# Performance work log

Measured on AMD Instinct MI355X. Metric: run time of the kernel, lower is better.

## Reference

```python
import jax, jax.numpy as jnp
import numpy as np

B, N, C = 8, 8192, 64
P, K = 2048, 16
C_IN = 2 * C + 6   # 134: concat(diff, center) of (feat ++ xyz)
H1, H2 = 64, 128
EPS = 1e-5


def setup_inputs() -> dict:
    key = jax.random.key(0)
    ks = jax.random.split(key, 16)
    inp = {
        "xyz": jax.random.normal(ks[0], (B, N, 3), dtype=jnp.float32),
        "feat": jax.random.normal(ks[1], (B, C, N), dtype=jnp.float32),
        # SharedMLP layer 1: 1x1 conv + BN(eval) + ReLU
        "W1": jax.random.normal(ks[2], (H1, C_IN), dtype=jnp.float32) * (1.0 / np.sqrt(C_IN)),
        "b1": jnp.zeros((H1,), dtype=jnp.float32),
        "g1": jax.random.uniform(ks[3], (H1,), minval=0.5, maxval=1.5, dtype=jnp.float32),
        "be1": jax.random.normal(ks[4], (H1,), dtype=jnp.float32) * 0.1,
        "m1": jax.random.normal(ks[5], (H1,), dtype=jnp.float32) * 0.1,
        "v1": jax.random.uniform(ks[6], (H1,), minval=0.5, maxval=1.5, dtype=jnp.float32),
        # SharedMLP layer 2
        "W2": jax.random.normal(ks[7], (H2, H1), dtype=jnp.float32) * (1.0 / np.sqrt(H1)),
        "b2": jnp.zeros((H2,), dtype=jnp.float32),
        "g2": jax.random.uniform(ks[8], (H2,), minval=0.5, maxval=1.5, dtype=jnp.float32),
        "be2": jax.random.normal(ks[9], (H2,), dtype=jnp.float32) * 0.1,
        "m2": jax.random.normal(ks[10], (H2,), dtype=jnp.float32) * 0.1,
        "v2": jax.random.uniform(ks[11], (H2,), minval=0.5, maxval=1.5, dtype=jnp.float32),
        "npoints": P,
    }
    return inp


def _mlp_layer(x, W, b, g, be, m, v):
    # x: [b,p,k,cin] -> 1x1 conv (einsum) + eval-mode BN + ReLU
    y = jnp.einsum("bpkc,oc->bpko", x, W) + b
    y = g * (y - m) * jax.lax.rsqrt(v + EPS) + be
    return jax.nn.relu(y)


def reference(xyz, feat, W1, b1, g1, be1, m1, v1, W2, b2, g2, be2, m2, v2, npoints):
    p = npoints
    # Range sampling: take first p points
    new_xyz = xyz[:, :p]                       # [b,p,3]
    feat_t = jnp.swapaxes(feat, 1, 2)          # [b,n,c]
    feat_x = jnp.concatenate([feat_t, xyz], axis=-1)   # [b,n,c+3] (use_xyz)
    new_feat_x = feat_x[:, :p]                 # [b,p,c+3]
    # KNN via squared euclidean distance, expanded form to avoid [b,p,n,3]
    sq_q = jnp.sum(new_xyz * new_xyz, axis=-1)           # [b,p]
    sq_r = jnp.sum(xyz * xyz, axis=-1)                   # [b,n]
    dots = jnp.einsum("bpd,bnd->bpn", new_xyz, xyz)      # [b,p,n]
    d2 = sq_q[:, :, None] + sq_r[:, None, :] - 2.0 * dots
    _, idx = jax.lax.top_k(-d2, K)             # [b,p,k] nearest (ascending dist)
    # Gather neighbor features: [b,p,k,c+3]
    knn_feat = jax.vmap(lambda f, i: f[i])(feat_x, idx)
    tiled = jnp.broadcast_to(new_feat_x[:, :, None, :], knn_feat.shape)
    edge = jnp.concatenate([knn_feat - tiled, tiled], axis=-1)  # [b,p,k,2c+6]
    h = _mlp_layer(edge, W1, b1, g1, be1, m1, v1)
    h = _mlp_layer(h, W2, b2, g2, be2, m2, v2)              # [b,p,k,H2]
    new_feat = jnp.swapaxes(jnp.max(h, axis=2), 1, 2)       # [b,H2,p]
    sample_idx = jnp.broadcast_to(jnp.arange(p, dtype=jnp.int32), (xyz.shape[0], p))
    return new_xyz, new_feat, sample_idx
```

## Files before the change

kernel.cpp:

```cpp
#include <hip/hip_runtime.h>
#include <hip/hip_bf16.h>

#define BB 8
#define NN 8192
#define CC 64
#define PP 2048
#define KK 16
#define H1 64
#define H2 128
#define K2PAD 72

typedef float  f32x4 __attribute__((ext_vector_type(4)));
typedef short  s16x8 __attribute__((ext_vector_type(8)));

#define OFF_FXT   0u
#define OFF_PTS4  17825792u
#define OFF_W1P   20971520u
#define OFF_W2P   20996096u
#define OFF_C1    21014528u
#define OFF_C2    21014784u

#define FLTMAX 3.402823466e+38f

static __device__ __forceinline__ unsigned short bf16b(float v) {
    __hip_bfloat16 h = __float2bfloat16(v);
    return *reinterpret_cast<unsigned short*>(&h);
}
static __device__ __forceinline__ unsigned pk2(float a, float b) {
    return ((unsigned)bf16b(b) << 16) | (unsigned)bf16b(a);
}
static __device__ __forceinline__ s16x8 as8(uint4 v) {
    union { uint4 u; s16x8 s; } x; x.u = v; return x.s;
}
#define LDS_FENCE() asm volatile("s_waitcnt lgkmcnt(0)" ::: "memory")

__global__ __launch_bounds__(512) void k1_prep(const float* __restrict__ xyz,
                                               const float* __restrict__ feat,
                                               unsigned* __restrict__ fxtb,
                                               float4* __restrict__ pts4,
                                               float* __restrict__ out0,
                                               float* __restrict__ out2,
                                               const float* __restrict__ W1, const float* __restrict__ b1,
                                               const float* __restrict__ g1, const float* __restrict__ be1,
                                               const float* __restrict__ m1, const float* __restrict__ v1,
                                               const float* __restrict__ W2, const float* __restrict__ b2,
                                               const float* __restrict__ g2, const float* __restrict__ be2,
                                               const float* __restrict__ m2, const float* __restrict__ v2,
                                               unsigned short* __restrict__ w1p,
                                               unsigned short* __restrict__ w2p,
                                               float* __restrict__ c1, float* __restrict__ c2) {
    __shared__ float tile[72][65];
    if (blockIdx.x < 256 && threadIdx.x < 85) {
        int i = blockIdx.x * 85 + threadIdx.x;
        if (i < 6144) {
            int n = i / 96, c = i - n * 96;
            float s = g1[n] * rsqrtf(v1[n] + 1e-5f);
            w1p[n * 192 + c] = bf16b((c < 67) ? W1[n * 134 + c] * s : 0.f);
        } else if (i < 12288) {
            int j = i - 6144;
            int n = j / 96, c = j - n * 96;
            float s = g1[n] * rsqrtf(v1[n] + 1e-5f);
            w1p[n * 192 + 96 + c] =
                bf16b((c < 67) ? (W1[n * 134 + 67 + c] - W1[n * 134 + c]) * s : 0.f);
        } else if (i < 21504) {
            int j = i - 12288;
            int o = j / 72, k = j - o * 72;
            float s = g2[o] * rsqrtf(v2[o] + 1e-5f);
            w2p[j] = bf16b((k < 64) ? W2[o * 64 + k] * s : 0.f);
        } else if (i < 21568) {
            int l = i - 21504;
            float s = g1[l] * rsqrtf(v1[l] + 1e-5f);
            c1[l] = s * (b1[l] - m1[l]) + be1[l];
        } else if (i < 21696) {
            int p = i - 21568;
            float s = g2[p] * rsqrtf(v2[p] + 1e-5f);
            c2[p] = s * (b2[p] - m2[p]) + be2[p];
        }
    }
    int b  = blockIdx.x >> 7;
    int n0 = (blockIdx.x & 127) * 64;
    int tx = threadIdx.x & 63, ty = threadIdx.x >> 6;
    for (int c = ty; c < 72; c += 8) {
        float v;
        if (c < 64)       v = feat[((size_t)b * 64 + c) * NN + n0 + tx];
        else if (c < 67)  v = xyz[((size_t)b * NN + n0 + tx) * 3 + (c - 64)];
        else              v = 0.f;
        tile[c][tx] = v;
    }
    __syncthreads();
    size_t base = ((size_t)b * NN + n0) * 36;
    for (int e = threadIdx.x; e < 64 * 36; e += 512) {
        int nl = e / 36, c = e - nl * 36;
        fxtb[base + e] = pk2(tile[2 * c][nl], tile[2 * c + 1][nl]);
    }
    if (threadIdx.x < 64) {
        int n = n0 + threadIdx.x;
        float x = tile[64][threadIdx.x], y = tile[65][threadIdx.x], z = tile[66][threadIdx.x];
        pts4[(size_t)b * NN + n] = make_float4(x, y, z, x * x + y * y + z * z);
        if (n0 < PP) out2[b * PP + n] = (float)n;
    }
    if (n0 < PP) {
        for (int e = threadIdx.x; e < 64 * 3; e += 512) {
            int nl = e / 3, d = e - nl * 3;
            out0[((size_t)b * PP + n0 + nl) * 3 + d] = tile[64 + d][nl];
        }
    }
}

__global__ __launch_bounds__(1024, 1) void k23(const float4* __restrict__ pts4,
                                               const unsigned* __restrict__ fxtb,
                                               const unsigned short* __restrict__ w1p,
                                               const unsigned short* __restrict__ w2p,
                                               const float* __restrict__ c1,
                                               const float* __restrict__ c2,
                                               float* __restrict__ out1) {
    __shared__ __align__(16) char smem[131072];
    __shared__ float2 scratch[16][2][64];
    __shared__ int knnl[16][64];
    int lane = threadIdx.x & 63;
    int wv   = threadIdx.x >> 6;
    int b    = blockIdx.x & 7;
    int q0base = (blockIdx.x >> 3) * 64;
    size_t pb = (size_t)b * NN;

    {
        float4* stage = (float4*)smem;
        int q0 = q0base + wv * 4;

        float4 qc = make_float4(0.f, 0.f, 0.f, 0.f);
        if (lane < 4) qc = pts4[pb + q0 + lane];
        float qx2 = -2.f * qc.x, qy2 = -2.f * qc.y, qz2 = -2.f * qc.z;
        float bx[4], by[4], bz[4];
#pragma unroll
        for (int q = 0; q < 4; ++q) {
            bx[q] = __shfl(qx2, q); by[q] = __shfl(qy2, q); bz[q] = __shfl(qz2, q);
        }

#pragma unroll
        for (int i = 0; i < 8; ++i) {
            int p = i * 1024 + threadIdx.x;
            float4 v = pts4[pb + p];
            int r = p >> 6, c = p & 63;
            stage[(r << 6) | ((c + (r >> 1)) & 63)] = v;
        }
        __syncthreads();

        float m[4];
#pragma unroll
        for (int q = 0; q < 4; ++q) m[q] = FLTMAX;
#pragma unroll
        for (int rr = 0; rr < 2; ++rr) {
            int rowbase = (2 * lane + rr) << 6;
#pragma unroll
            for (int j8 = 0; j8 < 8; ++j8) {
                float4 cc[8];
#pragma unroll
                for (int i = 0; i < 8; ++i)
                    cc[i] = stage[rowbase | ((j8 * 8 + i + lane) & 63)];
#pragma unroll
                for (int q = 0; q < 4; ++q) {
                    float x = bx[q], y = by[q], z = bz[q];
#pragma unroll
                    for (int i = 0; i < 8; i += 2) {
                        float e0 = fmaf(z, cc[i].z, fmaf(y, cc[i].y, fmaf(x, cc[i].x, cc[i].w)));
                        float e1 = fmaf(z, cc[i+1].z, fmaf(y, cc[i+1].y, fmaf(x, cc[i+1].x, cc[i+1].w)));
                        m[q] = fminf(fminf(m[q], e0), e1);
                    }
                }
            }
        }

        float sv0 = m[0], sv1 = m[1], sv2 = m[2], sv3 = m[3];
#pragma unroll
        for (int k = 2; k <= 64; k <<= 1) {
#pragma unroll
            for (int j = k >> 1; j > 0; j >>= 1) {
                bool keepMin = (((lane & k) == 0) == ((lane & j) == 0));
                float p0 = __shfl_xor(sv0, j, 64);
                float p1 = __shfl_xor(sv1, j, 64);
                float p2 = __shfl_xor(sv2, j, 64);
                float p3 = __shfl_xor(sv3, j, 64);
                sv0 = keepMin ? fminf(sv0, p0) : fmaxf(sv0, p0);
                sv1 = keepMin ? fminf(sv1, p1) : fmaxf(sv1, p1);
                sv2 = keepMin ? fminf(sv2, p2) : fmaxf(sv2, p2);
                sv3 = keepMin ? fminf(sv3, p3) : fmaxf(sv3, p3);
            }
        }
        float T[4];
        T[0] = __shfl(sv0, 15, 64); T[1] = __shfl(sv1, 15, 64);
        T[2] = __shfl(sv2, 15, 64); T[3] = __shfl(sv3, 15, 64);

        unsigned long long below = (lane == 63) ? 0x7FFFFFFFFFFFFFFFull
                                                : ((1ull << lane) - 1ull);
#pragma unroll
        for (int pr = 0; pr < 4; pr += 2) {
            int Ms[2];
#pragma unroll
            for (int u = 0; u < 2; ++u) {
                int q = pr + u;
                float x = bx[q], y = by[q], z = bz[q], tq = T[q];
                unsigned long long rm = __ballot(m[q] <= tq);
                int cnt = 0;
                while (rm) {
                    int sl = __ffsll((long long)rm) - 1; rm &= rm - 1;
                    int phys = (lane + sl) & 63;
                    float4 c0 = stage[((2 * sl) << 6) | phys];
                    float4 c1v_ = stage[((2 * sl + 1) << 6) | phys];
                    float e0 = fmaf(z, c0.z, fmaf(y, c0.y, fmaf(x, c0.x, c0.w)));
                    float e1 = fmaf(z, c1v_.z, fmaf(y, c1v_.y, fmaf(x, c1v_.x, c1v_.w)));
                    unsigned long long b0 = __ballot(e0 <= tq);
                    if (e0 <= tq) {
                        int pos = cnt + __popcll(b0 & below);
                        if (pos < 64)
                            scratch[wv][u][pos] = make_float2(e0, __int_as_float(sl * 128 + lane));
                    }
                    cnt += __popcll(b0);
                    unsigned long long b1 = __ballot(e1 <= tq);
                    if (e1 <= tq) {
                        int pos = cnt + __popcll(b1 & below);
                        if (pos < 64)
                            scratch[wv][u][pos] = make_float2(e1, __int_as_float(sl * 128 + 64 + lane));
                    }
                    cnt += __popcll(b1);
                }
                Ms[u] = min(cnt, 64);
            }
            LDS_FENCE();
#pragma unroll
            for (int u = 0; u < 2; ++u) {
                int M = Ms[u];
                float2 own = scratch[wv][u][lane];
                float di = own.x; int ni = __float_as_int(own.y);
                int rank = 0;
                const float2* buf = &scratch[wv][u][0];
#pragma unroll 4
                for (int j = 0; j < M; ++j) {
                    float2 e = buf[j];
                    int nj = __float_as_int(e.y);
                    rank += (e.x < di || (e.x == di && nj < ni)) ? 1 : 0;
                }
                if (lane < M && rank < 16)
                    knnl[wv][(pr + u) * 16 + rank] = ni;
            }
            LDS_FENCE();
        }
    }

    int idxAll = knnl[wv][lane];

    __syncthreads();

    unsigned short* w1a   = (unsigned short*)smem;
    unsigned short* w2l   = (unsigned short*)(smem + 13312);
    unsigned short* h1all = (unsigned short*)(smem + 35840);
    float*          otile = (float*)(smem + 72704);
    int col = lane & 15, quad = lane >> 4;
    const uint4* fx4 = (const uint4*)fxtb;
    size_t rowb = (size_t)b * NN;

    {
        const unsigned* src1 = (const unsigned*)w1p;
        unsigned* d1 = (unsigned*)w1a;
        for (int t = threadIdx.x; t < 64 * 48; t += 1024) {
            int r = t / 48, c = t - r * 48;
            d1[r * 52 + c] = src1[r * 96 + c];
        }
        const unsigned* src2 = (const unsigned*)w2p;
        unsigned* d2 = (unsigned*)w2l;
        for (int t = threadIdx.x; t < 128 * 36; t += 1024) {
            int r = t / 36, c = t - r * 36;
            d2[r * 44 + c] = src2[r * 36 + c];
        }
    }

    f32x4 accq[4];
#pragma unroll
    for (int nt = 0; nt < 4; ++nt) accq[nt] = (f32x4){0.f, 0.f, 0.f, 0.f};
    {
        const uint4* rp = fx4 + (rowb + q0base + wv * 4 + col) * 9;
        uint4 qf0 = rp[quad];
        uint4 qf1 = rp[4 + quad];
        uint4 qf2 = rp[8];
        if (quad != 0) qf2 = make_uint4(0u, 0u, 0u, 0u);
        uint4 qf[3] = {qf0, qf1, qf2};
#pragma unroll
        for (int ks = 0; ks < 3; ++ks) {
            s16x8 a = as8(qf[ks]);
#pragma unroll
            for (int nt = 0; nt < 4; ++nt) {
                s16x8 bfr = *(const s16x8*)(w1p + (nt * 16 + col) * 192 + 96 + ks * 32 + quad * 8);
                accq[nt] = __builtin_amdgcn_mfma_f32_16x16x32_bf16(a, bfr, accq[nt], 0, 0, 0);
            }
        }
    }
    float qcc[4][4];
    {
        float c1v[4];
#pragma unroll
        for (int nt = 0; nt < 4; ++nt) c1v[nt] = c1[nt * 16 + col];
#pragma unroll
        for (int qi = 0; qi < 4; ++qi)
#pragma unroll
            for (int nt = 0; nt < 4; ++nt)
                qcc[qi][nt] = __shfl(accq[nt][qi], col, 64) + c1v[nt];
    }
    float c2v[8];
#pragma unroll
    for (int nt = 0; nt < 8; ++nt) c2v[nt] = c2[nt * 16 + col];

    __syncthreads();

    unsigned short* h1w = h1all + wv * (16 * K2PAD);

    uint4 af[2][3];
#define PREF(buf, qi_) {                                                      \
        int nidx_ = __shfl(idxAll, (qi_) * 16 + col, 64);                     \
        const uint4* rp_ = fx4 + (rowb + nidx_) * 9;                          \
        af[buf][0] = rp_[quad];                                               \
        af[buf][1] = rp_[4 + quad];                                           \
        uint4 f2_ = rp_[8];                                                   \
        af[buf][2] = (quad == 0) ? f2_ : make_uint4(0u, 0u, 0u, 0u); }

    PREF(0, 0);

#pragma unroll
    for (int qi = 0; qi < 4; ++qi) {
        const int cur = qi & 1;
        f32x4 acc1[4];
#pragma unroll
        for (int nt = 0; nt < 4; ++nt)
            acc1[nt] = (f32x4){qcc[qi][nt], qcc[qi][nt], qcc[qi][nt], qcc[qi][nt]};
#pragma unroll
        for (int ks = 0; ks < 3; ++ks) {
            s16x8 a = as8(af[cur][ks]);
#pragma unroll
            for (int nt = 0; nt < 4; ++nt) {
                s16x8 bfr = *(const s16x8*)(w1a + (nt * 16 + col) * 104 + ks * 32 + quad * 8);
                acc1[nt] = __builtin_amdgcn_mfma_f32_16x16x32_bf16(a, bfr, acc1[nt], 0, 0, 0);
            }
        }
        if (qi < 3) PREF(cur ^ 1, qi + 1);
#pragma unroll
        for (int nt = 0; nt < 4; ++nt)
#pragma unroll
            for (int rr = 0; rr < 4; ++rr)
                h1w[(quad * 4 + rr) * K2PAD + nt * 16 + col] = bf16b(fmaxf(acc1[nt][rr], 0.f));
        LDS_FENCE();
#pragma unroll
        for (int hf = 0; hf < 2; ++hf) {
            f32x4 acc2[4];
#pragma unroll
            for (int nt = 0; nt < 4; ++nt) acc2[nt] = (f32x4){0.f, 0.f, 0.f, 0.f};
#pragma unroll
            for (int ks = 0; ks < 2; ++ks) {
                s16x8 a2 = *(const s16x8*)(h1w + col * K2PAD + ks * 32 + quad * 8);
#pragma unroll
                for (int nt = 0; nt < 4; ++nt) {
                    s16x8 wf = *(const s16x8*)(w2l + ((hf * 4 + nt) * 16 + col) * 88 + ks * 32 + quad * 8);
                    acc2[nt] = __builtin_amdgcn_mfma_f32_16x16x32_bf16(a2, wf, acc2[nt], 0, 0, 0);
                }
            }
#pragma unroll
            for (int nt = 0; nt < 4; ++nt) {
                float m0 = fmaxf(fmaxf(acc2[nt][0], acc2[nt][1]), fmaxf(acc2[nt][2], acc2[nt][3]));
                m0 = fmaxf(m0 + c2v[hf * 4 + nt], 0.f);
                m0 = fmaxf(m0, __shfl_xor(m0, 16, 64));
                m0 = fmaxf(m0, __shfl_xor(m0, 32, 64));
                if (quad == 0)
                    otile[(wv * 4 + qi) * 130 + (hf * 4 + nt) * 16 + col] = m0;
            }
        }
        LDS_FENCE();
    }
    __syncthreads();
    for (int i = threadIdx.x; i < H2 * 64; i += 1024) {
        int ch = i >> 6, q = i & 63;
        out1[((size_t)(b * H2 + ch)) * PP + q0base + q] = otile[q * 130 + ch];
    }
#undef PREF
}

extern "C" void kernel_launch(void* const* d_in, const int* in_sizes, int n_in,
                              void* d_out, int out_size, void* d_ws, size_t ws_size,
                              hipStream_t stream) {
    const float* xyz  = (const float*)d_in[0];
    const float* feat = (const float*)d_in[1];
    const float* W1   = (const float*)d_in[2];
    const float* b1   = (const float*)d_in[3];
    const float* g1   = (const float*)d_in[4];
    const float* be1  = (const float*)d_in[5];
    const float* m1   = (const float*)d_in[6];
    const float* v1   = (const float*)d_in[7];
    const float* W2   = (const float*)d_in[8];
    const float* b2   = (const float*)d_in[9];
    const float* g2   = (const float*)d_in[10];
    const float* be2  = (const float*)d_in[11];
    const float* m2   = (const float*)d_in[12];
    const float* v2   = (const float*)d_in[13];

    char* ws = (char*)d_ws;
    unsigned*       fxtb = (unsigned*)(ws + OFF_FXT);
    float4*         pts4 = (float4*)(ws + OFF_PTS4);
    unsigned short* w1p  = (unsigned short*)(ws + OFF_W1P);
    unsigned short* w2p  = (unsigned short*)(ws + OFF_W2P);
    float*          c1   = (float*)(ws + OFF_C1);
    float*          c2   = (float*)(ws + OFF_C2);

    float* out0 = (float*)d_out;
    float* out1 = out0 + (size_t)BB * PP * 3;
    float* out2 = out1 + (size_t)BB * H2 * PP;

    hipLaunchKernelGGL(k1_prep, dim3(1024), dim3(512), 0, stream,
                       xyz, feat, fxtb, pts4, out0, out2,
                       W1, b1, g1, be1, m1, v1, W2, b2, g2, be2, m2, v2,
                       w1p, w2p, c1, c2);
    hipLaunchKernelGGL(k23, dim3(256), dim3(1024), 0, stream,
                       pts4, fxtb, w1p, w2p, c1, c2, out1);
}
```

Baseline: 153.5 us.

## Fuse prep and KNN/MLP kernels into one cooperative kernel with grid sync

Merges the preprocessing kernel into the main KNN+MLP kernel, launched cooperatively with 256 blocks. Each block transposes and packs its share of features to bf16 and prepares weights, then runs KNN, and a grid-wide sync placed before the MLP phase guarantees the packed data is visible. The pts4 buffer is dropped; points and their squared norms are recomputed from xyz directly. The second-layer A fragments are also hoisted out of the hf loop. The aim is to remove one kernel launch and to overlap the prep work with the KNN phase, at the cost of cooperative-launch constraints, a grid barrier, and strided 3-float xyz loads.

```diff
diff --git a/kernel.cpp b/kernel.cpp
--- a/kernel.cpp
+++ b/kernel.cpp
@@ -1,5 +1,8 @@
 #include <hip/hip_runtime.h>
 #include <hip/hip_bf16.h>
+#include <hip/hip_cooperative_groups.h>
+
+namespace cg = cooperative_groups;
 
 #define BB 8
 #define NN 8192
@@ -14,7 +17,6 @@
 typedef short  s16x8 __attribute__((ext_vector_type(8)));
 
 #define OFF_FXT   0u
-#define OFF_PTS4  17825792u
 #define OFF_W1P   20971520u
 #define OFF_W2P   20996096u
 #define OFF_C1    21014528u
@@ -34,101 +36,96 @@
 }
 #define LDS_FENCE() asm volatile("s_waitcnt lgkmcnt(0)" ::: "memory")
 
-__global__ __launch_bounds__(512) void k1_prep(const float* __restrict__ xyz,
-                                               const float* __restrict__ feat,
-                                               unsigned* __restrict__ fxtb,
-                                               float4* __restrict__ pts4,
-                                               float* __restrict__ out0,
-                                               float* __restrict__ out2,
-                                               const float* __restrict__ W1, const float* __restrict__ b1,
-                                               const float* __restrict__ g1, const float* __restrict__ be1,
-                                               const float* __restrict__ m1, const float* __restrict__ v1,
-                                               const float* __restrict__ W2, const float* __restrict__ b2,
-                                               const float* __restrict__ g2, const float* __restrict__ be2,
-                                               const float* __restrict__ m2, const float* __restrict__ v2,
-                                               unsigned short* __restrict__ w1p,
-                                               unsigned short* __restrict__ w2p,
-                                               float* __restrict__ c1, float* __restrict__ c2) {
-    __shared__ float tile[72][65];
-    if (blockIdx.x < 256 && threadIdx.x < 85) {
-        int i = blockIdx.x * 85 + threadIdx.x;
-        if (i < 6144) {
-            int n = i / 96, c = i - n * 96;
-            float s = g1[n] * rsqrtf(v1[n] + 1e-5f);
-            w1p[n * 192 + c] = bf16b((c < 67) ? W1[n * 134 + c] * s : 0.f);
-        } else if (i < 12288) {
-            int j = i - 6144;
-            int n = j / 96, c = j - n * 96;
-            float s = g1[n] * rsqrtf(v1[n] + 1e-5f);
-            w1p[n * 192 + 96 + c] =
-                bf16b((c < 67) ? (W1[n * 134 + 67 + c] - W1[n * 134 + c]) * s : 0.f);
-        } else if (i < 21504) {
-            int j = i - 12288;
-            int o = j / 72, k = j - o * 72;
-            float s = g2[o] * rsqrtf(v2[o] + 1e-5f);
-            w2p[j] = bf16b((k < 64) ? W2[o * 64 + k] * s : 0.f);
-        } else if (i < 21568) {
-            int l = i - 21504;
-            float s = g1[l] * rsqrtf(v1[l] + 1e-5f);
-            c1[l] = s * (b1[l] - m1[l]) + be1[l];
-        } else if (i < 21696) {
-            int p = i - 21568;
-            float s = g2[p] * rsqrtf(v2[p] + 1e-5f);
-            c2[p] = s * (b2[p] - m2[p]) + be2[p];
-        }
-    }
-    int b  = blockIdx.x >> 7;
-    int n0 = (blockIdx.x & 127) * 64;
-    int tx = threadIdx.x & 63, ty = threadIdx.x >> 6;
-    for (int c = ty; c < 72; c += 8) {
-        float v;
-        if (c < 64)       v = feat[((size_t)b * 64 + c) * NN + n0 + tx];
-        else if (c < 67)  v = xyz[((size_t)b * NN + n0 + tx) * 3 + (c - 64)];
-        else              v = 0.f;
-        tile[c][tx] = v;
-    }
-    __syncthreads();
-    size_t base = ((size_t)b * NN + n0) * 36;
-    for (int e = threadIdx.x; e < 64 * 36; e += 512) {
-        int nl = e / 36, c = e - nl * 36;
-        fxtb[base + e] = pk2(tile[2 * c][nl], tile[2 * c + 1][nl]);
-    }
-    if (threadIdx.x < 64) {
-        int n = n0 + threadIdx.x;
-        float x = tile[64][threadIdx.x], y = tile[65][threadIdx.x], z = tile[66][threadIdx.x];
-        pts4[(size_t)b * NN + n] = make_float4(x, y, z, x * x + y * y + z * z);
-        if (n0 < PP) out2[b * PP + n] = (float)n;
-    }
-    if (n0 < PP) {
-        for (int e = threadIdx.x; e < 64 * 3; e += 512) {
-            int nl = e / 3, d = e - nl * 3;
-            out0[((size_t)b * PP + n0 + nl) * 3 + d] = tile[64 + d][nl];
-        }
-    }
-}
-
-__global__ __launch_bounds__(1024, 1) void k23(const float4* __restrict__ pts4,
-                                               const unsigned* __restrict__ fxtb,
-                                               const unsigned short* __restrict__ w1p,
-                                               const unsigned short* __restrict__ w2p,
-                                               const float* __restrict__ c1,
-                                               const float* __restrict__ c2,
-                                               float* __restrict__ out1) {
+__global__ __launch_bounds__(1024, 1) void kfused(
+    const float* __restrict__ xyz,  const float* __restrict__ feat,
+    const float* __restrict__ W1,   const float* __restrict__ b1,
+    const float* __restrict__ g1,   const float* __restrict__ be1,
+    const float* __restrict__ m1,   const float* __restrict__ v1,
+    const float* __restrict__ W2,   const float* __restrict__ b2,
+    const float* __restrict__ g2,   const float* __restrict__ be2,
+    const float* __restrict__ m2,   const float* __restrict__ v2,
+    unsigned* __restrict__ fxtb,    unsigned short* __restrict__ w1p,
+    unsigned short* __restrict__ w2p, float* __restrict__ c1,
+    float* __restrict__ c2,
+    float* __restrict__ out0, float* __restrict__ out1, float* __restrict__ out2) {
+
     __shared__ __align__(16) char smem[131072];
     __shared__ float2 scratch[16][2][64];
     __shared__ int knnl[16][64];
     int lane = threadIdx.x & 63;
     int wv   = threadIdx.x >> 6;
     int b    = blockIdx.x & 7;
-    int q0base = (blockIdx.x >> 3) * 64;
+    int g    = blockIdx.x >> 3;
+    int q0base = g * 64;
     size_t pb = (size_t)b * NN;
+
+    {
+        float (*tile)[72][65] = (float (*)[72][65])smem;
+        int grp = threadIdx.x >> 8;
+        int t256 = threadIdx.x & 255;
+        int tx = t256 & 63, ty = t256 >> 6;
+        int n0 = (g * 4 + grp) * 64;
+        for (int c = ty; c < 72; c += 4) {
+            float v;
+            if (c < 64)       v = feat[((size_t)b * 64 + c) * NN + n0 + tx];
+            else if (c < 67)  v = xyz[((size_t)b * NN + n0 + tx) * 3 + (c - 64)];
+            else              v = 0.f;
+            tile[grp][c][tx] = v;
+        }
+        if (threadIdx.x < 85) {
+            int i = blockIdx.x * 85 + threadIdx.x;
+            if (i < 6144) {
+                int n = i / 96, c = i - n * 96;
+                float s = g1[n] * rsqrtf(v1[n] + 1e-5f);
+                w1p[n * 192 + c] = bf16b((c < 67) ? W1[n * 134 + c] * s : 0.f);
+            } else if (i < 12288) {
+                int j = i - 6144;
+                int n = j / 96, c = j - n * 96;
+                float s = g1[n] * rsqrtf(v1[n] + 1e-5f);
+                w1p[n * 192 + 96 + c] =
+                    bf16b((c < 67) ? (W1[n * 134 + 67 + c] - W1[n * 134 + c]) * s : 0.f);
+            } else if (i < 21504) {
+                int j = i - 12288;
+                int o = j / 72, k = j - o * 72;
+                float s = g2[o] * rsqrtf(v2[o] + 1e-5f);
+                w2p[j] = bf16b((k < 64) ? W2[o * 64 + k] * s : 0.f);
+            } else if (i < 21568) {
+                int l = i - 21504;
+                float s = g1[l] * rsqrtf(v1[l] + 1e-5f);
+                c1[l] = s * (b1[l] - m1[l]) + be1[l];
+            } else if (i < 21696) {
+                int p = i - 21568;
+                float s = g2[p] * rsqrtf(v2[p] + 1e-5f);
+                c2[p] = s * (b2[p] - m2[p]) + be2[p];
+            }
+        }
+        __syncthreads();
+        size_t base = ((size_t)b * NN + n0) * 36;
+        for (int e = t256; e < 64 * 36; e += 256) {
+            int nl = e / 36, c = e - nl * 36;
+            fxtb[base + e] = pk2(tile[grp][2 * c][nl], tile[grp][2 * c + 1][nl]);
+        }
+        if (n0 < PP) {
+            if (t256 < 64)
+                out2[b * PP + n0 + t256] = (float)(n0 + t256);
+            for (int e = t256; e < 64 * 3; e += 256) {
+                int nl = e / 3, d = e - nl * 3;
+                out0[((size_t)b * PP + n0 + nl) * 3 + d] = tile[grp][64 + d][nl];
+            }
+        }
+        __syncthreads();
+    }
 
     {
         float4* stage = (float4*)smem;
         int q0 = q0base + wv * 4;
 
         float4 qc = make_float4(0.f, 0.f, 0.f, 0.f);
-        if (lane < 4) qc = pts4[pb + q0 + lane];
+        if (lane < 4) {
+            const float* qp = xyz + (pb + q0 + lane) * 3;
+            float x = qp[0], y = qp[1], z = qp[2];
+            qc = make_float4(x, y, z, x * x + y * y + z * z);
+        }
         float qx2 = -2.f * qc.x, qy2 = -2.f * qc.y, qz2 = -2.f * qc.z;
         float bx[4], by[4], bz[4];
 #pragma unroll
@@ -139,9 +136,11 @@
 #pragma unroll
         for (int i = 0; i < 8; ++i) {
             int p = i * 1024 + threadIdx.x;
-            float4 v = pts4[pb + p];
+            const float* pp = xyz + (pb + p) * 3;
+            float x = pp[0], y = pp[1], z = pp[2];
             int r = p >> 6, c = p & 63;
-            stage[(r << 6) | ((c + (r >> 1)) & 63)] = v;
+            stage[(r << 6) | ((c + (r >> 1)) & 63)] =
+                make_float4(x, y, z, x * x + y * y + z * z);
         }
         __syncthreads();
 
@@ -248,7 +247,7 @@
 
     int idxAll = knnl[wv][lane];
 
-    __syncthreads();
+    cg::this_grid().sync();
 
     unsigned short* w1a   = (unsigned short*)smem;
     unsigned short* w2l   = (unsigned short*)(smem + 13312);
@@ -346,6 +345,9 @@
             for (int rr = 0; rr < 4; ++rr)
                 h1w[(quad * 4 + rr) * K2PAD + nt * 16 + col] = bf16b(fmaxf(acc1[nt][rr], 0.f));
         LDS_FENCE();
+        s16x8 a2f[2];
+        a2f[0] = *(const s16x8*)(h1w + col * K2PAD + quad * 8);
+        a2f[1] = *(const s16x8*)(h1w + col * K2PAD + 32 + quad * 8);
 #pragma unroll
         for (int hf = 0; hf < 2; ++hf) {
             f32x4 acc2[4];
@@ -353,11 +355,10 @@
             for (int nt = 0; nt < 4; ++nt) acc2[nt] = (f32x4){0.f, 0.f, 0.f, 0.f};
 #pragma unroll
             for (int ks = 0; ks < 2; ++ks) {
-                s16x8 a2 = *(const s16x8*)(h1w + col * K2PAD + ks * 32 + quad * 8);
 #pragma unroll
                 for (int nt = 0; nt < 4; ++nt) {
                     s16x8 wf = *(const s16x8*)(w2l + ((hf * 4 + nt) * 16 + col) * 88 + ks * 32 + quad * 8);
-                    acc2[nt] = __builtin_amdgcn_mfma_f32_16x16x32_bf16(a2, wf, acc2[nt], 0, 0, 0);
+                    acc2[nt] = __builtin_amdgcn_mfma_f32_16x16x32_bf16(a2f[ks], wf, acc2[nt], 0, 0, 0);
                 }
             }
 #pragma unroll
@@ -400,7 +401,6 @@
 
     char* ws = (char*)d_ws;
     unsigned*       fxtb = (unsigned*)(ws + OFF_FXT);
-    float4*         pts4 = (float4*)(ws + OFF_PTS4);
     unsigned short* w1p  = (unsigned short*)(ws + OFF_W1P);
     unsigned short* w2p  = (unsigned short*)(ws + OFF_W2P);
     float*          c1   = (float*)(ws + OFF_C1);
@@ -410,10 +410,13 @@
     float* out1 = out0 + (size_t)BB * PP * 3;
     float* out2 = out1 + (size_t)BB * H2 * PP;
 
-    hipLaunchKernelGGL(k1_prep, dim3(1024), dim3(512), 0, stream,
-                       xyz, feat, fxtb, pts4, out0, out2,
-                       W1, b1, g1, be1, m1, v1, W2, b2, g2, be2, m2, v2,
-                       w1p, w2p, c1, c2);
-    hipLaunchKernelGGL(k23, dim3(256), dim3(1024), 0, stream,
-                       pts4, fxtb, w1p, w2p, c1, c2, out1);
+    void* args[] = {
+        (void*)&xyz, (void*)&feat,
+        (void*)&W1, (void*)&b1, (void*)&g1, (void*)&be1, (void*)&m1, (void*)&v1,
+        (void*)&W2, (void*)&b2, (void*)&g2, (void*)&be2, (void*)&m2, (void*)&v2,
+        (void*)&fxtb, (void*)&w1p, (void*)&w2p, (void*)&c1, (void*)&c2,
+        (void*)&out0, (void*)&out1, (void*)&out2
+    };
+    hipLaunchCooperativeKernel(reinterpret_cast<const void*>(kfused),
+                               dim3(256), dim3(1024), args, 0u, stream);
 }
```

Result: slower. 206.4 us (+34.5%).

## Restage KNN candidate points as SoA pairs and use packed FMA distance evaluation

Applied to the files above, without the earlier changes.

Point coordinates for the brute-force KNN scan are restaged into two LDS arrays that interleave pairs of points component-wise, so each distance pair is computed with v_pk_fma_f32 and reduced with v_min3_f32. This targets the VALU cost of the distance scan, which dominates the kernel. The h1 tile stride changes from 72 to 76 to avoid LDS bank conflicts, and the layer-2 A fragments are hoisted out of the hf loop. The change adds inline asm and a new LDS layout, and the refinement pass has to decode the same layout.

```diff
diff --git a/kernel.cpp b/kernel.cpp
--- a/kernel.cpp
+++ b/kernel.cpp
@@ -8,9 +8,10 @@
 #define KK 16
 #define H1 64
 #define H2 128
-#define K2PAD 72
+#define H1STR 76
 
 typedef float  f32x4 __attribute__((ext_vector_type(4)));
+typedef float  f32x2 __attribute__((ext_vector_type(2)));
 typedef short  s16x8 __attribute__((ext_vector_type(8)));
 
 #define OFF_FXT   0u
@@ -124,7 +125,8 @@
     size_t pb = (size_t)b * NN;
 
     {
-        float4* stage = (float4*)smem;
+        float4* stageA = (float4*)smem;
+        float4* stageB = (float4*)(smem + 65536);
         int q0 = q0base + wv * 4;
 
         float4 qc = make_float4(0.f, 0.f, 0.f, 0.f);
@@ -137,35 +139,48 @@
         }
 
 #pragma unroll
-        for (int i = 0; i < 8; ++i) {
+        for (int i = 0; i < 4; ++i) {
             int p = i * 1024 + threadIdx.x;
-            float4 v = pts4[pb + p];
             int r = p >> 6, c = p & 63;
-            stage[(r << 6) | ((c + (r >> 1)) & 63)] = v;
+            float4 e0 = pts4[pb + r * 128 + c];
+            float4 e1 = pts4[pb + r * 128 + 64 + c];
+            int s = (r << 6) | ((c + r) & 63);
+            stageA[s] = make_float4(e0.x, e1.x, e0.y, e1.y);
+            stageB[s] = make_float4(e0.z, e1.z, e0.w, e1.w);
         }
         __syncthreads();
 
         float m[4];
-#pragma unroll
-        for (int q = 0; q < 4; ++q) m[q] = FLTMAX;
-#pragma unroll
-        for (int rr = 0; rr < 2; ++rr) {
-            int rowbase = (2 * lane + rr) << 6;
-#pragma unroll
-            for (int j8 = 0; j8 < 8; ++j8) {
-                float4 cc[8];
-#pragma unroll
-                for (int i = 0; i < 8; ++i)
-                    cc[i] = stage[rowbase | ((j8 * 8 + i + lane) & 63)];
-#pragma unroll
-                for (int q = 0; q < 4; ++q) {
-                    float x = bx[q], y = by[q], z = bz[q];
-#pragma unroll
-                    for (int i = 0; i < 8; i += 2) {
-                        float e0 = fmaf(z, cc[i].z, fmaf(y, cc[i].y, fmaf(x, cc[i].x, cc[i].w)));
-                        float e1 = fmaf(z, cc[i+1].z, fmaf(y, cc[i+1].y, fmaf(x, cc[i+1].x, cc[i+1].w)));
-                        m[q] = fminf(fminf(m[q], e0), e1);
-                    }
+        f32x2 bx2[4], by2[4], bz2[4];
+#pragma unroll
+        for (int q = 0; q < 4; ++q) {
+            m[q] = FLTMAX;
+            bx2[q] = (f32x2){bx[q], bx[q]};
+            by2[q] = (f32x2){by[q], by[q]};
+            bz2[q] = (f32x2){bz[q], bz[q]};
+        }
+        int rbase = lane << 6;
+#pragma unroll
+        for (int jj = 0; jj < 16; ++jj) {
+            float4 A[4], Bv[4];
+#pragma unroll
+            for (int i = 0; i < 4; ++i) {
+                int phys = (jj * 4 + i + lane) & 63;
+                A[i]  = stageA[rbase | phys];
+                Bv[i] = stageB[rbase | phys];
+            }
+#pragma unroll
+            for (int q = 0; q < 4; ++q) {
+#pragma unroll
+                for (int i = 0; i < 4; ++i) {
+                    f32x2 e  = (f32x2){Bv[i].z, Bv[i].w};
+                    f32x2 xs = (f32x2){A[i].x, A[i].y};
+                    f32x2 ys = (f32x2){A[i].z, A[i].w};
+                    f32x2 zs = (f32x2){Bv[i].x, Bv[i].y};
+                    asm("v_pk_fma_f32 %0, %1, %2, %0" : "+v"(e) : "v"(bx2[q]), "v"(xs));
+                    asm("v_pk_fma_f32 %0, %1, %2, %0" : "+v"(e) : "v"(by2[q]), "v"(ys));
+                    asm("v_pk_fma_f32 %0, %1, %2, %0" : "+v"(e) : "v"(bz2[q]), "v"(zs));
+                    asm("v_min3_f32 %0, %0, %1, %2" : "+v"(m[q]) : "v"(e.x), "v"(e.y));
                 }
             }
         }
@@ -203,11 +218,11 @@
                 int cnt = 0;
                 while (rm) {
                     int sl = __ffsll((long long)rm) - 1; rm &= rm - 1;
-                    int phys = (lane + sl) & 63;
-                    float4 c0 = stage[((2 * sl) << 6) | phys];
-                    float4 c1v_ = stage[((2 * sl + 1) << 6) | phys];
-                    float e0 = fmaf(z, c0.z, fmaf(y, c0.y, fmaf(x, c0.x, c0.w)));
-                    float e1 = fmaf(z, c1v_.z, fmaf(y, c1v_.y, fmaf(x, c1v_.x, c1v_.w)));
+                    int s = (sl << 6) | ((lane + sl) & 63);
+                    float4 A = stageA[s];
+                    float4 Bv = stageB[s];
+                    float e0 = fmaf(z, Bv.x, fmaf(y, A.z, fmaf(x, A.x, Bv.z)));
+                    float e1 = fmaf(z, Bv.y, fmaf(y, A.w, fmaf(x, A.y, Bv.w)));
                     unsigned long long b0 = __ballot(e0 <= tq);
                     if (e0 <= tq) {
                         int pos = cnt + __popcll(b0 & below);
@@ -251,9 +266,9 @@
     __syncthreads();
 
     unsigned short* w1a   = (unsigned short*)smem;
-    unsigned short* w2l   = (unsigned short*)(smem + 13312);
-    unsigned short* h1all = (unsigned short*)(smem + 35840);
-    float*          otile = (float*)(smem + 72704);
+    unsigned short* h1all = (unsigned short*)(smem + 13312);
+    unsigned short* w2l   = (unsigned short*)(smem + 52224);
+    float*          otile = (float*)(smem + 74752);
     int col = lane & 15, quad = lane >> 4;
     const uint4* fx4 = (const uint4*)fxtb;
     size_t rowb = (size_t)b * NN;
@@ -310,7 +325,7 @@
 
     __syncthreads();
 
-    unsigned short* h1w = h1all + wv * (16 * K2PAD);
+    unsigned short* h1w = h1all + wv * (16 * H1STR);
 
     uint4 af[2][3];
 #define PREF(buf, qi_) {                                                      \
@@ -344,8 +359,11 @@
         for (int nt = 0; nt < 4; ++nt)
 #pragma unroll
             for (int rr = 0; rr < 4; ++rr)
-                h1w[(quad * 4 + rr) * K2PAD + nt * 16 + col] = bf16b(fmaxf(acc1[nt][rr], 0.f));
+                h1w[(quad * 4 + rr) * H1STR + nt * 16 + col] = bf16b(fmaxf(acc1[nt][rr], 0.f));
         LDS_FENCE();
+        s16x8 a2f[2];
+        a2f[0] = *(const s16x8*)(h1w + col * H1STR + quad * 8);
+        a2f[1] = *(const s16x8*)(h1w + col * H1STR + 32 + quad * 8);
 #pragma unroll
         for (int hf = 0; hf < 2; ++hf) {
             f32x4 acc2[4];
@@ -353,11 +371,10 @@
             for (int nt = 0; nt < 4; ++nt) acc2[nt] = (f32x4){0.f, 0.f, 0.f, 0.f};
 #pragma unroll
             for (int ks = 0; ks < 2; ++ks) {
-                s16x8 a2 = *(const s16x8*)(h1w + col * K2PAD + ks * 32 + quad * 8);
 #pragma unroll
                 for (int nt = 0; nt < 4; ++nt) {
                     s16x8 wf = *(const s16x8*)(w2l + ((hf * 4 + nt) * 16 + col) * 88 + ks * 32 + quad * 8);
-                    acc2[nt] = __builtin_amdgcn_mfma_f32_16x16x32_bf16(a2, wf, acc2[nt], 0, 0, 0);
+                    acc2[nt] = __builtin_amdgcn_mfma_f32_16x16x32_bf16(a2f[ks], wf, acc2[nt], 0, 0, 0);
                 }
             }
 #pragma unroll
```

Result: slower. 161.3 us (+5.1%).
